# Optimization experiments

Measured on AMD Instinct MI355X. Metric: run time of the kernel, lower is better.

Reference implementation:

```python
import jax, jax.numpy as jnp
import numpy as np
from jax import lax

THR = 0.0
NMS_SIZE = 5
PAD = NMS_SIZE // 2
B, C, H, W = 8, 1, 2048, 2048
# Upper bound on number of surviving peaks: ~1/(2*25) of pixels pass in
# expectation for iid noise; B*H*W//8 is a very safe static cap.
MAX_PEAKS = (B * H * W) // 8


def max_filter(x):
    # torch MaxPool2d(kernel=5, stride=1, padding=2) == max reduce_window
    # with -inf padding, same spatial output shape.
    return lax.reduce_window(
        x, -jnp.inf, lax.max,
        window_dimensions=(1, 1, NMS_SIZE, NMS_SIZE),
        window_strides=(1, 1, 1, 1),
        padding=[(0, 0), (0, 0), (PAD, PAD), (PAD, PAD)],
    )


def setup_inputs() -> dict:
    key = jax.random.key(0)
    scores = jax.random.normal(key, (B, C, H, W), dtype=jnp.float32)
    return {"scores": scores}


def reference(scores):
    # maxima = (scores == maxpool(scores)) & (scores > thr)
    maxima = (scores == max_filter(scores)) & (scores > THR)
    # torch: maxima.nonzero().t()[2:4] -> [2, K] rows = (h, w) coords.
    # jit-safe: fixed-size nonzero, padded with -1 for absent entries.
    idx = jnp.nonzero(maxima, size=MAX_PEAKS, fill_value=-1)
    return jnp.stack([idx[2], idx[3]])  # [2, MAX_PEAKS]
```

## Files before the change

kernel.cpp:

```cpp
#include <hip/hip_runtime.h>
#include <math.h>

#define IMG_W 2048
#define IMG_H 2048
#define BATCH 8
#define MAX_PEAKS ((BATCH * IMG_H * IMG_W) / 8)
#define NWORDS (BATCH * IMG_H * IMG_W / 32)
#define ROWSW 32
#define NFILL 2048

__device__ __forceinline__ void load_row(const float* __restrict__ colp,
                                         const float* __restrict__ ecolp,
                                         int gr, bool leftHalf, bool evalid,
                                         float4& nv, float2& ne) {
    const float NEG = -INFINITY;
    int rc = gr < 0 ? 0 : (gr > IMG_H - 1 ? IMG_H - 1 : gr);
    size_t off = (size_t)rc * IMG_W;
    float4 v = *(const float4*)(colp + off);
    float4 ev = *(const float4*)(ecolp + off);
    bool rv = ((unsigned)gr < IMG_H);
    bool ok = rv && evalid;
    float ex = leftHalf ? ev.z : ev.x;
    float ey = leftHalf ? ev.w : ev.y;
    nv.x = rv ? v.x : NEG;
    nv.y = rv ? v.y : NEG;
    nv.z = rv ? v.z : NEG;
    nv.w = rv ? v.w : NEG;
    ne.x = ok ? ex : NEG;
    ne.y = ok ? ey : NEG;
}

__global__ __launch_bounds__(256, 4) void nms_mask(const float* __restrict__ scores,
                                                   unsigned* __restrict__ words,
                                                   unsigned* __restrict__ bsum2) {
    const int t = threadIdx.x;
    const int lane = t & 63;
    const int wv = t >> 6;
    const int b = blockIdx.x;
    const int img = b >> 7;
    const int rem = b & 127;
    const int strip = rem >> 4;
    const int chunk = rem & 15;
    const int r0 = chunk * 128 + wv * ROWSW;
    const int c0 = strip * 256;
    const int cl = c0 + lane * 4;
    const size_t imgBase = (size_t)img * (IMG_H * IMG_W);

    const float* colp = scores + imgBase + cl;
    const bool leftHalf = (lane < 32);
    const bool isL = (lane == 0), isR = (lane == 63);
    int ecol = leftHalf ? (c0 - 4) : (c0 + 256);
    const bool evalid = ((unsigned)ecol < IMG_W);
    int ecolC = evalid ? ecol : c0;
    const float* ecolp = scores + imgBase + ecolC;

    float4 ring[8];
    float2 ringE[8];

#pragma unroll
    for (int m = 0; m < 4; ++m)
        load_row(colp, ecolp, r0 - 2 + m, leftHalf, evalid, ring[m], ringE[m]);

    unsigned cnt = 0;
    const int shamt = (lane & 7) * 4;
    size_t wIdx = (size_t)(img * IMG_H + r0) * (IMG_W / 32) + strip * 8 + (lane >> 3);
    const int cb0 = (img * IMG_H + r0) >> 4;

#pragma unroll 1
    for (int i8 = 0; i8 < ROWSW / 8; ++i8) {
#pragma unroll
        for (int u = 0; u < 8; ++u) {
            const int gr = r0 + i8 * 8 + u + 2;
            load_row(colp, ecolp, gr, leftHalf, evalid,
                     ring[(u + 4) & 7], ringE[(u + 4) & 7]);

            const float4 w0 = ring[u & 7];
            const float4 w1 = ring[(u + 1) & 7];
            const float4 mid = ring[(u + 2) & 7];
            const float4 w3 = ring[(u + 3) & 7];
            const float4 w4 = ring[(u + 4) & 7];
            float vmx = fmaxf(fmaxf(fmaxf(w0.x, w1.x), fmaxf(mid.x, w3.x)), w4.x);
            float vmy = fmaxf(fmaxf(fmaxf(w0.y, w1.y), fmaxf(mid.y, w3.y)), w4.y);
            float vmz = fmaxf(fmaxf(fmaxf(w0.z, w1.z), fmaxf(mid.z, w3.z)), w4.z);
            float vmw = fmaxf(fmaxf(fmaxf(w0.w, w1.w), fmaxf(mid.w, w3.w)), w4.w);
            const float2 e0 = ringE[u & 7];
            const float2 e1 = ringE[(u + 1) & 7];
            const float2 e2 = ringE[(u + 2) & 7];
            const float2 e3 = ringE[(u + 3) & 7];
            const float2 e4 = ringE[(u + 4) & 7];
            float vex = fmaxf(fmaxf(fmaxf(e0.x, e1.x), fmaxf(e2.x, e3.x)), e4.x);
            float vey = fmaxf(fmaxf(fmaxf(e0.y, e1.y), fmaxf(e2.y, e3.y)), e4.y);

            float A = __shfl_up(vmz, 1);
            float B = __shfl_up(vmw, 1);
            float C = __shfl_down(vmx, 1);
            float D = __shfl_down(vmy, 1);
            if (isL) { A = vex; B = vey; }
            if (isR) { C = vex; D = vey; }

            float t12 = fmaxf(vmy, vmz);
            float m02 = fmaxf(vmx, t12);
            float m03 = fmaxf(m02, vmw);
            float m13 = fmaxf(t12, vmw);
            float h0 = fmaxf(fmaxf(A, B), m02);
            float h1 = fmaxf(B, m03);
            float h2 = fmaxf(m03, C);
            float h3 = fmaxf(m13, fmaxf(C, D));

            unsigned nib = 0;
            nib |= (mid.x > 0.0f && mid.x >= h0) ? 1u : 0u;
            nib |= (mid.y > 0.0f && mid.y >= h1) ? 2u : 0u;
            nib |= (mid.z > 0.0f && mid.z >= h2) ? 4u : 0u;
            nib |= (mid.w > 0.0f && mid.w >= h3) ? 8u : 0u;

            unsigned wd = nib << shamt;
            wd |= __shfl_xor(wd, 1);
            wd |= __shfl_xor(wd, 2);
            wd |= __shfl_xor(wd, 4);
            if ((lane & 7) == 0) {
                words[wIdx] = wd;
                cnt += __popc(wd);
            }
            wIdx += IMG_W / 32;
        }
        if (i8 & 1) {
            unsigned s = cnt;
            s += __shfl_xor(s, 1);
            s += __shfl_xor(s, 2);
            s += __shfl_xor(s, 4);
            s += __shfl_xor(s, 8);
            s += __shfl_xor(s, 16);
            s += __shfl_xor(s, 32);
            if (lane == 0) bsum2[(cb0 + (i8 >> 1)) * 8 + strip] = s;
            cnt = 0;
        }
    }
}

__global__ __launch_bounds__(256) void nms_scan(const unsigned* __restrict__ bsum2,
                                                unsigned* __restrict__ base) {
    __shared__ unsigned wtot[4];
    const int t = threadIdx.x;
    const int lane = t & 63, wid = t >> 6;
    const uint4* p = (const uint4*)(bsum2 + t * 32);
    unsigned c[4];
#pragma unroll
    for (int i = 0; i < 4; ++i) {
        uint4 a = p[2 * i], bq = p[2 * i + 1];
        c[i] = a.x + a.y + a.z + a.w + bq.x + bq.y + bq.z + bq.w;
    }
    unsigned s0 = c[0], s1 = s0 + c[1], s2 = s1 + c[2], ts = s2 + c[3];
    unsigned sc = ts;
#pragma unroll
    for (int d = 1; d < 64; d <<= 1) {
        unsigned o = __shfl_up(sc, d);
        if (lane >= d) sc += o;
    }
    if (lane == 63) wtot[wid] = sc;
    __syncthreads();
    unsigned wpre = 0;
#pragma unroll
    for (int k = 0; k < 4; ++k) wpre += (k < wid) ? wtot[k] : 0u;
    unsigned excl = wpre + sc - ts;
    ((uint4*)base)[t] = make_uint4(excl, excl + s0, excl + s1, excl + s2);
    if (t == 255) base[1024] = wpre + sc;
}

__global__ __launch_bounds__(256) void nms_compact(const unsigned* __restrict__ words,
                                                   const unsigned* __restrict__ base,
                                                   int* __restrict__ out) {
    const int t = threadIdx.x;
    const int b = blockIdx.x;
    if (b < 1024) {
        __shared__ unsigned wq[4];
        const int lane = t & 63, wid = t >> 6;
        uint4 q = ((const uint4*)(words + b * 1024))[t];
        unsigned wv[4] = {q.x, q.y, q.z, q.w};
        unsigned tsum = __popc(wv[0]) + __popc(wv[1]) + __popc(wv[2]) + __popc(wv[3]);
        unsigned sc = tsum;
#pragma unroll
        for (int d = 1; d < 64; d <<= 1) {
            unsigned o = __shfl_up(sc, d);
            if (lane >= d) sc += o;
        }
        if (lane == 63) wq[wid] = sc;
        __syncthreads();
        unsigned wpre = 0;
#pragma unroll
        for (int k = 0; k < 4; ++k) wpre += (k < wid) ? wq[k] : 0u;
        unsigned off = base[b] + wpre + sc - tsum;

        const unsigned gword0 = (unsigned)b * 1024u + (unsigned)t * 4u;
#pragma unroll
        for (int wi = 0; wi < 4; ++wi) {
            unsigned m = wv[wi];
            unsigned pbase = (gword0 + wi) << 5;
            while (m) {
                int bit = __builtin_ctz(m);
                m &= m - 1;
                unsigned ppix = pbase + (unsigned)bit;
                int hh = (int)((ppix >> 11) & 2047u);
                int ww = (int)(ppix & 2047u);
                if (off < (unsigned)MAX_PEAKS) {
                    out[off] = hh;
                    out[MAX_PEAKS + off] = ww;
                }
                ++off;
            }
        }
    } else {
        unsigned total = base[1024];
        if (total > (unsigned)MAX_PEAKS) total = MAX_PEAKS;
        unsigned tail = (unsigned)MAX_PEAKS - total;
        unsigned fb = (unsigned)(b - 1024);
        unsigned per = (tail + NFILL - 1) / NFILL;
        unsigned s = total + fb * per;
        unsigned e = s + per;
        if (e > (unsigned)MAX_PEAKS) e = MAX_PEAKS;
        for (unsigned k = s + t; k < e; k += 256) {
            out[k] = -1;
            out[MAX_PEAKS + k] = -1;
        }
    }
}

extern "C" void kernel_launch(void* const* d_in, const int* in_sizes, int n_in,
                              void* d_out, int out_size, void* d_ws, size_t ws_size,
                              hipStream_t stream) {
    const float* scores = (const float*)d_in[0];
    int* out = (int*)d_out;
    unsigned* words = (unsigned*)d_ws;
    unsigned* bsum2 = words + NWORDS;
    unsigned* base = bsum2 + 8192;

    nms_mask<<<1024, 256, 0, stream>>>(scores, words, bsum2);
    nms_scan<<<1, 256, 0, stream>>>(bsum2, base);
    nms_compact<<<1024 + NFILL, 256, 0, stream>>>(words, base, out);
}
```

Before: 212.4 us.

## Deepen row prefetch, narrow edge loads, and vectorize tail fill

The mask kernel now keeps seven rows in flight in the register ring instead of four, and interior strips advance plain pointers without clamping or masking. Halo column loads shrink from float4 to float2 reads of only the two needed edge values. The fill phase of the compact kernel writes -1 with aligned int4 stores plus scalar head and tail pieces. These changes target load latency, address arithmetic and store count, at the cost of more registers and a duplicated slow path for boundary rows.

```diff
diff --git a/kernel.cpp b/kernel.cpp
--- a/kernel.cpp
+++ b/kernel.cpp
@@ -9,26 +9,99 @@
 #define ROWSW 32
 #define NFILL 2048
 
-__device__ __forceinline__ void load_row(const float* __restrict__ colp,
-                                         const float* __restrict__ ecolp,
-                                         int gr, bool leftHalf, bool evalid,
-                                         float4& nv, float2& ne) {
-    const float NEG = -INFINITY;
-    int rc = gr < 0 ? 0 : (gr > IMG_H - 1 ? IMG_H - 1 : gr);
-    size_t off = (size_t)rc * IMG_W;
-    float4 v = *(const float4*)(colp + off);
-    float4 ev = *(const float4*)(ecolp + off);
-    bool rv = ((unsigned)gr < IMG_H);
-    bool ok = rv && evalid;
-    float ex = leftHalf ? ev.z : ev.x;
-    float ey = leftHalf ? ev.w : ev.y;
-    nv.x = rv ? v.x : NEG;
-    nv.y = rv ? v.y : NEG;
-    nv.z = rv ? v.z : NEG;
-    nv.w = rv ? v.w : NEG;
-    ne.x = ok ? ex : NEG;
-    ne.y = ok ? ey : NEG;
-}
+
+#define NMS_COMPUTE(uu)                                                       \
+  {                                                                           \
+    const float4 w0 = ring[(uu) & 7];                                         \
+    const float4 w1 = ring[((uu) + 1) & 7];                                   \
+    const float4 mid = ring[((uu) + 2) & 7];                                  \
+    const float4 w3 = ring[((uu) + 3) & 7];                                   \
+    const float4 w4 = ring[((uu) + 4) & 7];                                   \
+    float vmx = fmaxf(fmaxf(fmaxf(w0.x, w1.x), fmaxf(mid.x, w3.x)), w4.x);    \
+    float vmy = fmaxf(fmaxf(fmaxf(w0.y, w1.y), fmaxf(mid.y, w3.y)), w4.y);    \
+    float vmz = fmaxf(fmaxf(fmaxf(w0.z, w1.z), fmaxf(mid.z, w3.z)), w4.z);    \
+    float vmw = fmaxf(fmaxf(fmaxf(w0.w, w1.w), fmaxf(mid.w, w3.w)), w4.w);    \
+    const float2 e0 = ringE[(uu) & 7];                                        \
+    const float2 e1 = ringE[((uu) + 1) & 7];                                  \
+    const float2 e2 = ringE[((uu) + 2) & 7];                                  \
+    const float2 e3 = ringE[((uu) + 3) & 7];                                  \
+    const float2 e4 = ringE[((uu) + 4) & 7];                                  \
+    float vex = fmaxf(fmaxf(fmaxf(e0.x, e1.x), fmaxf(e2.x, e3.x)), e4.x);     \
+    float vey = fmaxf(fmaxf(fmaxf(e0.y, e1.y), fmaxf(e2.y, e3.y)), e4.y);     \
+    float Av = __shfl_up(vmz, 1);                                             \
+    float Bv = __shfl_up(vmw, 1);                                             \
+    float Cv = __shfl_down(vmx, 1);                                           \
+    float Dv = __shfl_down(vmy, 1);                                           \
+    if (isL) { Av = vex; Bv = vey; }                                          \
+    if (isR) { Cv = vex; Dv = vey; }                                          \
+    float t12 = fmaxf(vmy, vmz);                                              \
+    float m02 = fmaxf(vmx, t12);                                              \
+    float m03 = fmaxf(m02, vmw);                                              \
+    float m13 = fmaxf(t12, vmw);                                              \
+    float h0 = fmaxf(fmaxf(Av, Bv), m02);                                     \
+    float h1 = fmaxf(Bv, m03);                                                \
+    float h2 = fmaxf(m03, Cv);                                                \
+    float h3 = fmaxf(m13, fmaxf(Cv, Dv));                                     \
+    unsigned nib = 0;                                                         \
+    nib |= (mid.x > 0.0f && mid.x >= h0) ? 1u : 0u;                           \
+    nib |= (mid.y > 0.0f && mid.y >= h1) ? 2u : 0u;                           \
+    nib |= (mid.z > 0.0f && mid.z >= h2) ? 4u : 0u;                           \
+    nib |= (mid.w > 0.0f && mid.w >= h3) ? 8u : 0u;                           \
+    unsigned wd = nib << shamt;                                               \
+    wd |= __shfl_xor(wd, 1);                                                  \
+    wd |= __shfl_xor(wd, 2);                                                  \
+    wd |= __shfl_xor(wd, 4);                                                  \
+    if ((lane & 7) == 0) {                                                    \
+      words[wIdx] = wd;                                                       \
+      cnt += __popc(wd);                                                      \
+    }                                                                         \
+    wIdx += IMG_W / 32;                                                       \
+  }
+
+#define PF_FAST(uu)                                                           \
+  {                                                                           \
+    ring[((uu) + 7) & 7] = *(const float4*)p;                                 \
+    const float2 _e = *(const float2*)pe;                                     \
+    float2 _ne;                                                               \
+    _ne.x = evalid ? _e.x : NEG;                                              \
+    _ne.y = evalid ? _e.y : NEG;                                              \
+    ringE[((uu) + 7) & 7] = _ne;                                              \
+    p += IMG_W;                                                               \
+    pe += IMG_W;                                                              \
+  }
+
+#define PF_SLOW(uu, gr)                                                       \
+  {                                                                           \
+    const int _rc = (gr) < 0 ? 0 : ((gr) > IMG_H - 1 ? IMG_H - 1 : (gr));     \
+    const size_t _off = (size_t)_rc * IMG_W;                                  \
+    const float4 _v = *(const float4*)(colp + _off);                          \
+    const float2 _e = *(const float2*)(ecolp + _off);                         \
+    const bool _rv = ((unsigned)(gr) < (unsigned)IMG_H);                      \
+    const bool _ok = _rv && evalid;                                           \
+    float4 _nv;                                                               \
+    float2 _ne;                                                               \
+    _nv.x = _rv ? _v.x : NEG;                                                 \
+    _nv.y = _rv ? _v.y : NEG;                                                 \
+    _nv.z = _rv ? _v.z : NEG;                                                 \
+    _nv.w = _rv ? _v.w : NEG;                                                 \
+    _ne.x = _ok ? _e.x : NEG;                                                 \
+    _ne.y = _ok ? _e.y : NEG;                                                 \
+    ring[((uu) + 7) & 7] = _nv;                                               \
+    ringE[((uu) + 7) & 7] = _ne;                                              \
+  }
+
+#define FLUSH(k)                                                              \
+  {                                                                           \
+    unsigned s = cnt;                                                         \
+    s += __shfl_xor(s, 1);                                                    \
+    s += __shfl_xor(s, 2);                                                    \
+    s += __shfl_xor(s, 4);                                                    \
+    s += __shfl_xor(s, 8);                                                    \
+    s += __shfl_xor(s, 16);                                                   \
+    s += __shfl_xor(s, 32);                                                   \
+    if (lane == 0) bsum2[(cb0 + (k)) * 8 + strip] = s;                        \
+    cnt = 0;                                                                  \
+  }
 
 __global__ __launch_bounds__(256, 4) void nms_mask(const float* __restrict__ scores,
                                                    unsigned* __restrict__ words,
@@ -44,95 +117,77 @@
     const int r0 = chunk * 128 + wv * ROWSW;
     const int c0 = strip * 256;
     const int cl = c0 + lane * 4;
-    const size_t imgBase = (size_t)img * (IMG_H * IMG_W);
+    const size_t imgBase = (size_t)img * ((size_t)IMG_H * IMG_W);
+    const float NEG = -INFINITY;
 
     const float* colp = scores + imgBase + cl;
     const bool leftHalf = (lane < 32);
     const bool isL = (lane == 0), isR = (lane == 63);
-    int ecol = leftHalf ? (c0 - 4) : (c0 + 256);
-    const bool evalid = ((unsigned)ecol < IMG_W);
-    int ecolC = evalid ? ecol : c0;
-    const float* ecolp = scores + imgBase + ecolC;
+    const int ecol2 = leftHalf ? (c0 - 2) : (c0 + 256);
+    const bool evalid = ((unsigned)ecol2 < (unsigned)IMG_W);
+    const int ecol2C = evalid ? ecol2 : c0;
+    const float* ecolp = scores + imgBase + ecol2C;
 
     float4 ring[8];
     float2 ringE[8];
-
-#pragma unroll
-    for (int m = 0; m < 4; ++m)
-        load_row(colp, ecolp, r0 - 2 + m, leftHalf, evalid, ring[m], ringE[m]);
 
     unsigned cnt = 0;
     const int shamt = (lane & 7) * 4;
     size_t wIdx = (size_t)(img * IMG_H + r0) * (IMG_W / 32) + strip * 8 + (lane >> 3);
     const int cb0 = (img * IMG_H + r0) >> 4;
 
+    const bool rowsInterior = (r0 >= 2) && (r0 + 33 <= IMG_H - 1);
+
+    if (rowsInterior) {
+        const float* p = colp + (size_t)(r0 - 2) * IMG_W;
+        const float* pe = ecolp + (size_t)(r0 - 2) * IMG_W;
+#pragma unroll
+        for (int m = 0; m < 7; ++m) {
+            ring[m] = *(const float4*)p;
+            const float2 _e = *(const float2*)pe;
+            ringE[m].x = evalid ? _e.x : NEG;
+            ringE[m].y = evalid ? _e.y : NEG;
+            p += IMG_W;
+            pe += IMG_W;
+        }
 #pragma unroll 1
-    for (int i8 = 0; i8 < ROWSW / 8; ++i8) {
-#pragma unroll
-        for (int u = 0; u < 8; ++u) {
-            const int gr = r0 + i8 * 8 + u + 2;
-            load_row(colp, ecolp, gr, leftHalf, evalid,
-                     ring[(u + 4) & 7], ringE[(u + 4) & 7]);
-
-            const float4 w0 = ring[u & 7];
-            const float4 w1 = ring[(u + 1) & 7];
-            const float4 mid = ring[(u + 2) & 7];
-            const float4 w3 = ring[(u + 3) & 7];
-            const float4 w4 = ring[(u + 4) & 7];
-            float vmx = fmaxf(fmaxf(fmaxf(w0.x, w1.x), fmaxf(mid.x, w3.x)), w4.x);
-            float vmy = fmaxf(fmaxf(fmaxf(w0.y, w1.y), fmaxf(mid.y, w3.y)), w4.y);
-            float vmz = fmaxf(fmaxf(fmaxf(w0.z, w1.z), fmaxf(mid.z, w3.z)), w4.z);
-            float vmw = fmaxf(fmaxf(fmaxf(w0.w, w1.w), fmaxf(mid.w, w3.w)), w4.w);
-            const float2 e0 = ringE[u & 7];
-            const float2 e1 = ringE[(u + 1) & 7];
-            const float2 e2 = ringE[(u + 2) & 7];
-            const float2 e3 = ringE[(u + 3) & 7];
-            const float2 e4 = ringE[(u + 4) & 7];
-            float vex = fmaxf(fmaxf(fmaxf(e0.x, e1.x), fmaxf(e2.x, e3.x)), e4.x);
-            float vey = fmaxf(fmaxf(fmaxf(e0.y, e1.y), fmaxf(e2.y, e3.y)), e4.y);
-
-            float A = __shfl_up(vmz, 1);
-            float B = __shfl_up(vmw, 1);
-            float C = __shfl_down(vmx, 1);
-            float D = __shfl_down(vmy, 1);
-            if (isL) { A = vex; B = vey; }
-            if (isR) { C = vex; D = vey; }
-
-            float t12 = fmaxf(vmy, vmz);
-            float m02 = fmaxf(vmx, t12);
-            float m03 = fmaxf(m02, vmw);
-            float m13 = fmaxf(t12, vmw);
-            float h0 = fmaxf(fmaxf(A, B), m02);
-            float h1 = fmaxf(B, m03);
-            float h2 = fmaxf(m03, C);
-            float h3 = fmaxf(m13, fmaxf(C, D));
-
-            unsigned nib = 0;
-            nib |= (mid.x > 0.0f && mid.x >= h0) ? 1u : 0u;
-            nib |= (mid.y > 0.0f && mid.y >= h1) ? 2u : 0u;
-            nib |= (mid.z > 0.0f && mid.z >= h2) ? 4u : 0u;
-            nib |= (mid.w > 0.0f && mid.w >= h3) ? 8u : 0u;
-
-            unsigned wd = nib << shamt;
-            wd |= __shfl_xor(wd, 1);
-            wd |= __shfl_xor(wd, 2);
-            wd |= __shfl_xor(wd, 4);
-            if ((lane & 7) == 0) {
-                words[wIdx] = wd;
-                cnt += __popc(wd);
+        for (int i8 = 0; i8 < 2; ++i8) {
+#pragma unroll
+            for (int uu = 0; uu < 8; ++uu) {
+                PF_FAST(uu);
+                NMS_COMPUTE(uu);
             }
-            wIdx += IMG_W / 32;
-        }
-        if (i8 & 1) {
-            unsigned s = cnt;
-            s += __shfl_xor(s, 1);
-            s += __shfl_xor(s, 2);
-            s += __shfl_xor(s, 4);
-            s += __shfl_xor(s, 8);
-            s += __shfl_xor(s, 16);
-            s += __shfl_xor(s, 32);
-            if (lane == 0) bsum2[(cb0 + (i8 >> 1)) * 8 + strip] = s;
-            cnt = 0;
+        }
+        FLUSH(0);
+#pragma unroll
+        for (int uu = 0; uu < 8; ++uu) {
+            PF_FAST(uu);
+            NMS_COMPUTE(uu);
+        }
+#pragma unroll
+        for (int uu = 0; uu < 5; ++uu) {
+            PF_FAST(uu);
+            NMS_COMPUTE(uu);
+        }
+#pragma unroll
+        for (int uu = 5; uu < 8; ++uu) {
+            NMS_COMPUTE(uu);
+        }
+        FLUSH(1);
+    } else {
+#pragma unroll
+        for (int m = 0; m < 7; ++m) {
+            PF_SLOW(m - 7, r0 - 2 + m);
+        }
+#pragma unroll 1
+        for (int i8 = 0; i8 < 4; ++i8) {
+#pragma unroll
+            for (int uu = 0; uu < 8; ++uu) {
+                const int U = i8 * 8 + uu;
+                PF_SLOW(uu, r0 + U + 5);
+                NMS_COMPUTE(uu);
+            }
+            if (i8 & 1) FLUSH(i8 >> 1);
         }
     }
 }
@@ -216,10 +271,24 @@
         unsigned per = (tail + NFILL - 1) / NFILL;
         unsigned s = total + fb * per;
         unsigned e = s + per;
+        if (s > (unsigned)MAX_PEAKS) s = MAX_PEAKS;
         if (e > (unsigned)MAX_PEAKS) e = MAX_PEAKS;
-        for (unsigned k = s + t; k < e; k += 256) {
-            out[k] = -1;
-            out[MAX_PEAKS + k] = -1;
+        unsigned a = (s + 3u) & ~3u;
+        if (a > e) a = e;
+        unsigned e4 = e & ~3u;
+        if (e4 < a) e4 = a;
+        if ((unsigned)t < a - s) {
+            out[s + t] = -1;
+            out[MAX_PEAKS + s + t] = -1;
+        }
+        const int4 m4 = make_int4(-1, -1, -1, -1);
+        for (unsigned k = a / 4 + t; k < e4 / 4; k += 256) {
+            ((int4*)out)[k] = m4;
+            ((int4*)(out + MAX_PEAKS))[k] = m4;
+        }
+        if ((unsigned)t < e - e4) {
+            out[e4 + t] = -1;
+            out[MAX_PEAKS + e4 + t] = -1;
         }
     }
 }
```

New measurement: 213.4 us. Within noise of the previous version (+0.5%).
